# Performance work log

Hardware: AMD Instinct MI355X
Metric: run time of the kernel (lower is better)

Reference implementation:

```python
import jax, jax.numpy as jnp
import numpy as np

KR = 3  # kernel_range, SHIFT = 1


def _neighborhood(x):
    """x: [B,H,W,C] -> [B,H,W,9,C] stacking the 3x3 shifted views (zero pad),
    in the same (i,j) raster order as the original loop."""
    B, H, W, C = x.shape
    xp = jnp.pad(x, ((0, 0), (1, 1), (1, 1), (0, 0)))
    views = [xp[:, 1 + i:1 + i + H, 1 + j:1 + j + W, :]
             for i in (-1, 0, 1) for j in (-1, 0, 1)]
    return jnp.stack(views, axis=3)


def _conv(x, w, b):
    # tf.nn.conv2d NHWC, HWIO, SAME, stride 1
    return jax.lax.conv_general_dilated(
        x, w, window_strides=(1, 1), padding='SAME',
        dimension_numbers=('NHWC', 'HWIO', 'NHWC')) + b


def setup_inputs() -> dict:
    key = jax.random.key(0)
    ks = jax.random.split(key, 10)
    B, H, W, D = 8, 128, 128, 64
    g = lambda k, shape, fan: jax.random.normal(k, shape, jnp.float32) * np.float32(1.0 / np.sqrt(fan))
    return {
        'x': jax.random.normal(ks[0], (B, H, W, D), jnp.float32),
        'Q_P': g(ks[1], (D, D), D),
        'K_P': g(ks[2], (D, D), D),
        'V_P': g(ks[3], (D, D), D),
        'ff1_kernel': g(ks[4], (3, 3, D, D), 9 * D),
        'ff1_bias': jax.random.normal(ks[5], (D,), jnp.float32) * 0.01,
        'ff2_kernel': g(ks[6], (3, 3, D, 2 * D), 9 * D),
        'ff2_bias': jax.random.normal(ks[7], (2 * D,), jnp.float32) * 0.01,
        'ff3_kernel': g(ks[8], (3, 3, 2 * D, D), 9 * 2 * D),
        'ff3_bias': jax.random.normal(ks[9], (D,), jnp.float32) * 0.01,
    }


def reference(x, Q_P, K_P, V_P, ff1_kernel, ff1_bias, ff2_kernel, ff2_bias,
              ff3_kernel, ff3_bias):
    B, H, W, D = x.shape
    # 3x3 neighborhood gather (zero padded) and validity mask
    stk = _neighborhood(x)                                   # [B,H,W,9,D]
    mask = _neighborhood(jnp.ones((B, H, W, 1), x.dtype))    # [B,H,W,9,1]
    mask = mask[..., 0]                                      # [B,H,W,9]

    q = jnp.einsum('bhwd,de->bhwe', x, Q_P)                  # [B,H,W,D]
    k = jnp.einsum('bhwkd,de->bhwke', stk, K_P)              # [B,H,W,9,D]
    v = jnp.einsum('bhwkd,de->bhwke', stk, V_P)              # [B,H,W,9,D]

    # NOTE: faithful to original -- scores are MULTIPLIED by the mask
    # (masked entries become 0, not -inf) before softmax over the 9 neighbors.
    scores = jnp.einsum('bhwke,bhwe->bhwk', k, q) * mask     # [B,H,W,9]
    alpha = jax.nn.softmax(scores, axis=-1)
    attn = jnp.einsum('bhwk,bhwke->bhwe', alpha, v)          # [B,H,W,D]

    t = x + attn
    t_in = t
    t = jax.nn.relu(_conv(t, ff1_kernel, ff1_bias))
    t = jax.nn.relu(_conv(t, ff2_kernel, ff2_bias))
    t = jax.nn.relu(_conv(t, ff3_kernel, ff3_bias))
    return t_in + t
```

## Files before the change

### kernel.cpp

```cpp
#include <hip/hip_runtime.h>

typedef unsigned int uint32;
typedef unsigned short u16;
typedef short s16x8 __attribute__((ext_vector_type(8)));
typedef short s16x4 __attribute__((ext_vector_type(4)));
typedef float f32x4 __attribute__((ext_vector_type(4)));

#define DEVINL static __device__ __forceinline__
#define MFMA16(a, b, c) __builtin_amdgcn_mfma_f32_16x16x32_bf16(a, b, c, 0, 0, 0)

DEVINL float bf2f(u16 u){ return __uint_as_float(((uint32)u) << 16); }
DEVINL u16 f2bf(float f){
  uint32 u = __float_as_uint(f);
  u += 0x7fffu + ((u >> 16) & 1u);
  return (u16)(u >> 16);
}
DEVINL uint32 pack2(float a, float b){
  return (uint32)f2bf(a) | (((uint32)f2bf(b)) << 16);
}

__global__ void detect_k(const uint32* __restrict__ x, uint32* __restrict__ flag){
  const int lane = threadIdx.x;
  int sane = 0;
  for (int i = 0; i < 32; ++i){
    uint32 u = x[i * 64 + lane];
    uint32 e = (u >> 7) & 0xffu;
    sane += (e >= 100u && e <= 150u) ? 1 : 0;
  }
  for (int off = 32; off >= 1; off >>= 1) sane += __shfl_xor(sane, off);
  if (lane == 0) *flag = (sane > 1024) ? 1u : 0u;
}

template<int M>
__global__ void cvtall_k(const void* s0, const void* s1, const void* s2,
                         const void* s3, const void* s4, const void* s5,
                         const void* s6, const void* s7, const void* s8,
                         float* __restrict__ wb, const uint32* __restrict__ flag)
{
  if (*flag != (uint32)M) return;
  const int i = blockIdx.x * 256 + threadIdx.x;
  if (i >= 196864) return;
  const void* s; int j;
  if      (i < 4096)   { s = s0; j = i; }
  else if (i < 8192)   { s = s1; j = i - 4096; }
  else if (i < 12288)  { s = s2; j = i - 8192; }
  else if (i < 49152)  { s = s3; j = i - 12288; }
  else if (i < 49216)  { s = s4; j = i - 49152; }
  else if (i < 122944) { s = s5; j = i - 49216; }
  else if (i < 123072) { s = s6; j = i - 122944; }
  else if (i < 196800) { s = s7; j = i - 123072; }
  else                 { s = s8; j = i - 196800; }
  wb[i] = M ? bf2f(((const u16*)s)[j]) : ((const float*)s)[j];
}

__global__ __launch_bounds__(256)
void xcvt_k(const void* __restrict__ x, u16* __restrict__ xb,
            const uint32* __restrict__ flag)
{
  if (*flag != 0u) return;
  const size_t i0 = ((size_t)blockIdx.x * 256 + threadIdx.x) * 8;
  const float4 f0 = ((const float4*)x)[i0 / 4];
  const float4 f1 = ((const float4*)x)[i0 / 4 + 1];
  uint4 o;
  o.x = pack2(f0.x, f0.y); o.y = pack2(f0.z, f0.w);
  o.z = pack2(f1.x, f1.y); o.w = pack2(f1.z, f1.w);
  *(uint4*)(xb + i0) = o;
}

__global__ void gcomp_k(const float* __restrict__ wb, u16* __restrict__ gt){
  const int t = blockIdx.x * 256 + threadIdx.x;
  const int d = t >> 6, c = t & 63;
  const float* __restrict__ K = wb + 4096;
  const float* __restrict__ Q = wb;
  float s = 0.f;
#pragma unroll
  for (int e = 0; e < 64; ++e) s = fmaf(K[d * 64 + e], Q[c * 64 + e], s);
  const u16 hi = f2bf(s);
  gt[t] = hi;
  gt[4096 + t] = f2bf(s - bf2f(hi));
}

__global__ void pack_k(const float* __restrict__ wb, u16* __restrict__ bb){
  int i = blockIdx.x * 256 + threadIdx.x;
  if (i < 4096){
    const int o = i >> 6, c = i & 63;
    bb[8192 + i] = f2bf(wb[8192 + c * 64 + o]);
    return;
  }
  i -= 4096;
  if (i < 4096){
    const int o = i >> 6, c = i & 63;
    const float v = wb[8192 + c * 64 + o];
    bb[12288 + i] = f2bf(v - bf2f(f2bf(v)));
    return;
  }
  i -= 4096;
  if (i < 36864){
    const int chunk = i >> 11, rr = i & 2047, co = rr >> 5, kkp = rr & 31;
    const int slot = (kkp >> 3) ^ ((co >> 1) & 3), kk = slot * 8 + (kkp & 7);
    const int tap = chunk >> 1, ci = (chunk & 1) * 32 + kk;
    bb[16384 + i] = f2bf(wb[12288 + (tap * 64 + ci) * 64 + co]);
    return;
  }
  i -= 36864;
  if (i < 73728){
    const int half = i / 36864, i2 = i - half * 36864;
    const int chunk = i2 >> 11, rr = i2 & 2047, co = rr >> 5, kkp = rr & 31;
    const int slot = (kkp >> 3) ^ ((co >> 1) & 3), kk = slot * 8 + (kkp & 7);
    const int tap = chunk >> 1, ci = (chunk & 1) * 32 + kk;
    bb[53248 + i] = f2bf(wb[49216 + (tap * 64 + ci) * 128 + half * 64 + co]);
    return;
  }
  i -= 73728;
  {
    const int chunk = i >> 11, rr = i & 2047, co = rr >> 5, kkp = rr & 31;
    const int slot = (kkp >> 3) ^ ((co >> 1) & 3), kk = slot * 8 + (kkp & 7);
    const int tap = chunk >> 2, ci = (chunk & 3) * 32 + kk;
    bb[126976 + i] = f2bf(wb[123072 + (tap * 128 + ci) * 64 + co]);
  }
}

template<int ROWS, int CIN, int STRIDE>
DEVINL void stage_tile(const u16* __restrict__ img_base, int h0, int w0, u16* lds){
  constexpr int CH8 = CIN / 8;
  constexpr int NCH = ROWS * 66 * CH8;
  for (int idx = threadIdx.x; idx < NCH; idx += 256){
    const int row  = idx / (66 * CH8);
    const int rem  = idx - row * 66 * CH8;
    const int col  = rem / CH8;
    const int slot = rem - col * CH8;
    const int hi = h0 + row - 1, wi = w0 + col - 1;
    uint4 v = make_uint4(0u, 0u, 0u, 0u);
    if (hi >= 0 && hi < 128 && wi >= 0 && wi < 128)
      v = *(const uint4*)(img_base + (size_t)(hi * 128 + wi) * STRIDE + slot * 8);
    const int dst = (row * 66 + col) * CIN + ((slot ^ (col & 7)) << 3);
    *(uint4*)(lds + dst) = v;
  }
}

template<int COUT_FULL, bool RES, int MOUT>
DEVINL void conv_epilogue(f32x4 acc[4][4], u16* xh, const u16* __restrict__ res,
                          void* __restrict__ out, int img, int h0, int w0, int co0,
                          int wv, int l15, int lk)
{
  float* tl = (float*)xh;
  const int lane = threadIdx.x & 63;
#pragma unroll
  for (int pass = 0; pass < 2; ++pass){
    __syncthreads();
#pragma unroll
    for (int at2 = 0; at2 < 2; ++at2){
      const int at = pass * 2 + at2;
      const int pp = wv * 32 + at2 * 16 + lk * 4;
#pragma unroll
      for (int nt = 0; nt < 4; ++nt)
#pragma unroll
        for (int reg = 0; reg < 4; ++reg)
          tl[(pp + reg) * 72 + nt * 16 + l15] = fmaxf(acc[at][nt][reg], 0.f);
    }
    __syncthreads();
    const size_t rowpx = (size_t)img * 16384 + (size_t)(h0 + wv) * 128 + w0 + pass * 32;
    if (MOUT == 0){
#pragma unroll
      for (int k = 0; k < 8; ++k){
        const int px = k * 4 + (lane >> 4);
        const int c4 = (lane & 15) * 4;
        float4 v = *(const float4*)(tl + (wv * 32 + px) * 72 + c4);
        if (RES){
          const uint2 r = *(const uint2*)(res + (rowpx + px) * 64 + c4);
          v.x += bf2f((u16)(r.x & 0xffff)); v.y += bf2f((u16)(r.x >> 16));
          v.z += bf2f((u16)(r.y & 0xffff)); v.w += bf2f((u16)(r.y >> 16));
        }
        *(float4*)((float*)out + (rowpx + px) * 64 + c4) = v;
      }
    } else {
#pragma unroll
      for (int k = 0; k < 4; ++k){
        const int px = k * 8 + (lane >> 3);
        const int c8 = (lane & 7) * 8;
        const float* tp = tl + (wv * 32 + px) * 72 + c8;
        const float4 a = *(const float4*)tp;
        const float4 b = *(const float4*)(tp + 4);
        float v0=a.x, v1=a.y, v2=a.z, v3=a.w, v4=b.x, v5=b.y, v6=b.z, v7=b.w;
        if (RES){
          const uint4 r = *(const uint4*)(res + (rowpx + px) * 64 + c8);
          v0 += bf2f((u16)(r.x & 0xffff)); v1 += bf2f((u16)(r.x >> 16));
          v2 += bf2f((u16)(r.y & 0xffff)); v3 += bf2f((u16)(r.y >> 16));
          v4 += bf2f((u16)(r.z & 0xffff)); v5 += bf2f((u16)(r.z >> 16));
          v6 += bf2f((u16)(r.w & 0xffff)); v7 += bf2f((u16)(r.w >> 16));
        }
        uint4 o;
        o.x = pack2(v0, v1); o.y = pack2(v2, v3);
        o.z = pack2(v4, v5); o.w = pack2(v6, v7);
        *(uint4*)((u16*)out + (rowpx + px) * COUT_FULL + co0 + c8) = o;
      }
    }
  }
}

__global__ __launch_bounds__(256, 4)
void attn_mfma(const u16* __restrict__ xraw, const u16* __restrict__ xcv,
               const u16* __restrict__ gt, const u16* __restrict__ vt,
               u16* __restrict__ tb, const uint32* __restrict__ flag)
{
  __shared__ __align__(16) u16 xh[3 * 66 * 64];
  u16* yl  = xh;
  u16* yl2 = xh + 2 * 66 * 64;
  const int bx0 = blockIdx.x;
  const int bx = (bx0 & 7) * 256 + (bx0 >> 3);
  const int img = bx >> 8, h = (bx >> 1) & 127, w0 = (bx & 1) * 64;
  const int p0 = img * 16384 + h * 128 + w0;
  const u16* __restrict__ xsrc = (*flag != 0u) ? xraw : xcv;
  stage_tile<3, 64, 64>(xsrc + (size_t)img * 16384 * 64, h, w0, xh);
  __syncthreads();

  const int lane = threadIdx.x & 63, wv = threadIdx.x >> 6;
  const int l15 = lane & 15, lk = lane >> 4;
  const int pxm = wv * 16 + l15;

  f32x4 racc[4];
#pragma unroll
  for (int nt = 0; nt < 4; ++nt) racc[nt] = (f32x4){0.f, 0.f, 0.f, 0.f};
#pragma unroll
  for (int half = 0; half < 2; ++half){
#pragma unroll
    for (int ks = 0; ks < 2; ++ks){
      const int colq = pxm + 1;
      const int slot = ks * 4 + lk;
      const s16x8 bx_ = *(const s16x8*)&xh[(66 + colq) * 64 + ((slot ^ (colq & 7)) << 3)];
#pragma unroll
      for (int nt = 0; nt < 4; ++nt){
        const s16x8 ag = *(const s16x8*)(gt + half * 4096 +
                          (size_t)(nt * 16 + l15) * 64 + ks * 32 + lk * 8);
        racc[nt] = MFMA16(ag, bx_, racc[nt]);
      }
    }
  }

  float sc[9];
#pragma unroll
  for (int n = 0; n < 9; ++n){
    const int tr = n / 3, tc = n % 3;
    const int col = pxm + tc;
    const u16* xr = &xh[(tr * 66 + col) * 64];
    float s = 0.f;
#pragma unroll
    for (int nt = 0; nt < 4; ++nt){
      const int slot = nt * 2 + (lk >> 1);
      const s16x4 v = *(const s16x4*)&xr[((slot ^ (col & 7)) << 3) + (lk & 1) * 4];
#pragma unroll
      for (int j = 0; j < 4; ++j)
        s = fmaf(bf2f((u16)v[j]), racc[nt][j], s);
    }
    sc[n] = s;
  }
#pragma unroll
  for (int n = 0; n < 9; ++n){
    sc[n] += __shfl_xor(sc[n], 16);
    sc[n] += __shfl_xor(sc[n], 32);
  }

  float mx = sc[0];
#pragma unroll
  for (int n = 1; n < 9; ++n) mx = fmaxf(mx, sc[n]);
  float sum = 0.f;
#pragma unroll
  for (int n = 0; n < 9; ++n){
    const float e = __expf(sc[n] - mx);
    sc[n] = e; sum += e;
  }
  const float inv = 1.f / sum;
#pragma unroll
  for (int n = 0; n < 9; ++n) sc[n] *= inv;

  float y[16];
#pragma unroll
  for (int j = 0; j < 16; ++j) y[j] = 0.f;
#pragma unroll
  for (int n = 0; n < 9; ++n){
    const int tr = n / 3, tc = n % 3;
    const int col = pxm + tc;
    const u16* xr = &xh[(tr * 66 + col) * 64];
    const float a = sc[n];
#pragma unroll
    for (int sl = 0; sl < 2; ++sl){
      const int slot = lk * 2 + sl;
      const s16x8 v = *(const s16x8*)&xr[(slot ^ (col & 7)) << 3];
#pragma unroll
      for (int j = 0; j < 8; ++j)
        y[sl * 8 + j] = fmaf(a, bf2f((u16)v[j]), y[sl * 8 + j]);
    }
  }

  __syncthreads();

#pragma unroll
  for (int sl = 0; sl < 2; ++sl){
    uint32 hwd[4], lwd[4];
#pragma unroll
    for (int j = 0; j < 4; ++j){
      const float a = y[sl * 8 + 2 * j], b = y[sl * 8 + 2 * j + 1];
      const u16 ha = f2bf(a), hb = f2bf(b);
      hwd[j] = (uint32)ha | ((uint32)hb << 16);
      lwd[j] = (uint32)f2bf(a - bf2f(ha)) | ((uint32)f2bf(b - bf2f(hb)) << 16);
    }
    const int slot = lk * 2 + sl;
    const int off = pxm * 64 + ((slot ^ (pxm & 7)) << 3);
    *(uint4*)&yl [off] = make_uint4(hwd[0], hwd[1], hwd[2], hwd[3]);
    *(uint4*)&yl2[off] = make_uint4(lwd[0], lwd[1], lwd[2], lwd[3]);
  }

  __syncthreads();

  f32x4 tacc[4];
#pragma unroll
  for (int nt = 0; nt < 4; ++nt) tacc[nt] = (f32x4){0.f, 0.f, 0.f, 0.f};
#pragma unroll
  for (int half = 0; half < 2; ++half){
    const u16* yb = half ? yl2 : yl;
#pragma unroll
    for (int ks = 0; ks < 2; ++ks){
      const int px = wv * 16 + l15;
      const int slot = ks * 4 + lk;
      const s16x8 af = *(const s16x8*)&yb[px * 64 + ((slot ^ (px & 7)) << 3)];
#pragma unroll
      for (int nt = 0; nt < 4; ++nt){
        const s16x8 bf = *(const s16x8*)(vt + (size_t)(nt * 16 + l15) * 64 + ks * 32 + lk * 8);
        tacc[nt] = MFMA16(af, bf, tacc[nt]);
      }
    }
  }
#pragma unroll
  for (int nt = 0; nt < 4; ++nt){
#pragma unroll
    for (int reg = 0; reg < 4; ++reg){
      const int pxo = wv * 16 + lk * 4 + reg;
      const int co = nt * 16 + l15;
      const int col = pxo + 1;
      const int elem = (66 + col) * 64 + (((co >> 3) ^ (col & 7)) << 3) + (co & 7);
      tb[(size_t)(p0 + pxo) * 64 + co] = f2bf(bf2f(xh[elem]) + tacc[nt][reg]);
    }
  }
}

template<int COUT_FULL, bool RES, int MOUT>
__global__ __launch_bounds__(256)
void conv_mfma(const u16* __restrict__ in, const u16* __restrict__ wpk,
               const float* __restrict__ bias, const u16* __restrict__ res,
               void* __restrict__ out, const uint32* __restrict__ flag)
{
  if (MOUT >= 0){ if (*flag != (uint32)MOUT) return; }
  constexpr int TOT = 18;
  __shared__ __align__(16) u16 xh[6 * 66 * 64];
  __shared__ __align__(16) u16 Bb[3][2048];

  const int bx0 = blockIdx.x;
  const int bx  = (bx0 & 7) * 64 + (bx0 >> 3);
  const int img = bx >> 6;
  const int rem = bx & 63;
  const int h0  = (rem >> 1) * 4;
  const int w0  = (rem & 1) * 64;
  const int co0 = blockIdx.y * 64;
  const u16* __restrict__ wp = wpk + (size_t)blockIdx.y * TOT * 2048;

  auto stageB = [&](int it, int buf){
    const char* g = (const char*)(wp + (size_t)it * 2048) + threadIdx.x * 16;
    char* l = (char*)&Bb[buf][0] + threadIdx.x * 16;
    __builtin_amdgcn_global_load_lds((const __attribute__((address_space(1))) void*)g,
                                     (__attribute__((address_space(3))) void*)l, 16, 0, 0);
  };

  stage_tile<6, 64, 64>(in + (size_t)img * 16384 * 64, h0, w0, xh);
  stageB(0, 0);
  stageB(1, 1);
  __syncthreads();

  const int lane = threadIdx.x & 63, wv = threadIdx.x >> 6;
  const int l15 = lane & 15, lk = lane >> 4;

  f32x4 acc[4][4];
#pragma unroll
  for (int nt = 0; nt < 4; ++nt){
    const float b = bias[co0 + nt * 16 + l15];
#pragma unroll
    for (int at = 0; at < 4; ++at) acc[at][nt] = (f32x4){b, b, b, b};
  }

#pragma unroll 1
  for (int it = 0; it < TOT; ++it){
    if (it + 2 < TOT) stageB(it + 2, (it + 2) % 3);
    const int b = it % 3;
    const int tap = it >> 1, ks = it & 1;
    const int tr = tap / 3, tc = tap - tr * 3;
    const int slot = ks * 4 + lk;
    s16x8 av[4], bv[4];
#pragma unroll
    for (int at = 0; at < 4; ++at){
      const int col = at * 16 + l15 + tc;
      av[at] = *(const s16x8*)&xh[((wv + tr) * 66 + col) * 64 + ((slot ^ (col & 7)) << 3)];
    }
#pragma unroll
    for (int nt = 0; nt < 4; ++nt){
      const int co = nt * 16 + l15;
      bv[nt] = *(const s16x8*)&Bb[b][co * 32 + ((lk ^ ((co >> 1) & 3)) << 3)];
    }
#pragma unroll
    for (int at = 0; at < 4; ++at)
#pragma unroll
      for (int nt = 0; nt < 4; ++nt)
        acc[at][nt] = MFMA16(av[at], bv[nt], acc[at][nt]);

    if (it + 1 < TOT){
      if (it + 2 < TOT) asm volatile("s_waitcnt vmcnt(1)" ::: "memory");
      else              asm volatile("s_waitcnt vmcnt(0)" ::: "memory");
      __builtin_amdgcn_s_barrier();
      __builtin_amdgcn_sched_barrier(0);
    }
  }

  conv_epilogue<COUT_FULL, RES, MOUT>(acc, xh, res, out, img, h0, w0, co0, wv, l15, lk);
}

template<int MOUT>
__global__ __launch_bounds__(256)
void conv3_mfma(const u16* __restrict__ in, const u16* __restrict__ wpk,
                const float* __restrict__ bias, const u16* __restrict__ res,
                void* __restrict__ out, const uint32* __restrict__ flag)
{
  if (*flag != (uint32)MOUT) return;
  __shared__ __align__(16) u16 xh[6 * 66 * 64];
  __shared__ __align__(16) u16 Bb[3][2048];

  const int bx0 = blockIdx.x;
  const int bx  = (bx0 & 7) * 64 + (bx0 >> 3);
  const int img = bx >> 6;
  const int rem = bx & 63;
  const int h0  = (rem >> 1) * 4;
  const int w0  = (rem & 1) * 64;

  auto stageB = [&](int chunk, int buf){
    const char* g = (const char*)(wpk + (size_t)chunk * 2048) + threadIdx.x * 16;
    char* l = (char*)&Bb[buf][0] + threadIdx.x * 16;
    __builtin_amdgcn_global_load_lds((const __attribute__((address_space(1))) void*)g,
                                     (__attribute__((address_space(3))) void*)l, 16, 0, 0);
  };

  const int lane = threadIdx.x & 63, wv = threadIdx.x >> 6;
  const int l15 = lane & 15, lk = lane >> 4;

  auto chunkOf = [&](int it, int half){
    return ((it >> 1) << 2) + half * 2 + (it & 1);
  };

  f32x4 acc[4][4];
#pragma unroll
  for (int nt = 0; nt < 4; ++nt){
    const float b = bias[nt * 16 + l15];
#pragma unroll
    for (int at = 0; at < 4; ++at) acc[at][nt] = (f32x4){b, b, b, b};
  }

#pragma unroll 1
  for (int half = 0; half < 2; ++half){
    if (half) __syncthreads();
    stage_tile<6, 64, 128>(in + (size_t)img * 16384 * 128 + half * 64, h0, w0, xh);
    stageB(chunkOf(0, half), 0);
    stageB(chunkOf(1, half), 1);
    __syncthreads();

#pragma unroll 1
    for (int it = 0; it < 18; ++it){
      if (it + 2 < 18) stageB(chunkOf(it + 2, half), (it + 2) % 3);
      const int b = it % 3;
      const int tap = it >> 1, ks2 = it & 1;
      const int tr = tap / 3, tc = tap - tr * 3;
      const int slot = ks2 * 4 + lk;
      s16x8 av[4], bv[4];
#pragma unroll
      for (int at = 0; at < 4; ++at){
        const int col = at * 16 + l15 + tc;
        av[at] = *(const s16x8*)&xh[((wv + tr) * 66 + col) * 64 + ((slot ^ (col & 7)) << 3)];
      }
#pragma unroll
      for (int nt = 0; nt < 4; ++nt){
        const int co = nt * 16 + l15;
        bv[nt] = *(const s16x8*)&Bb[b][co * 32 + ((lk ^ ((co >> 1) & 3)) << 3)];
      }
#pragma unroll
      for (int at = 0; at < 4; ++at)
#pragma unroll
        for (int nt = 0; nt < 4; ++nt)
          acc[at][nt] = MFMA16(av[at], bv[nt], acc[at][nt]);

      if (it + 1 < 18){
        if (it + 2 < 18) asm volatile("s_waitcnt vmcnt(1)" ::: "memory");
        else             asm volatile("s_waitcnt vmcnt(0)" ::: "memory");
        __builtin_amdgcn_s_barrier();
        __builtin_amdgcn_sched_barrier(0);
      }
    }
  }

  conv_epilogue<64, true, MOUT>(acc, xh, res, out, img, h0, w0, 0, wv, l15, lk);
}

extern "C" void kernel_launch(void* const* d_in, const int* in_sizes, int n_in,
                              void* d_out, int out_size, void* d_ws, size_t ws_size,
                              hipStream_t stream)
{
  (void)in_sizes; (void)n_in; (void)out_size; (void)ws_size;

  char* ws = (char*)d_ws;
  float*  wblob = (float*)ws;
  uint32* flag  = (uint32*)(ws + 983040);
  u16*    bb    = (u16*)(ws + (1u << 20));
  u16*    gt   = bb;
  u16*    vt   = bb + 8192;
  u16*    w1pk = bb + 16384;
  u16*    w2pk = bb + 53248;
  u16*    w3pk = bb + 126976;

  u16*   c2 = (u16*)(ws + (size_t)2097152);
  u16*   tb = (u16*)(ws + (size_t)35651584);
  u16*   xb = (u16*)(ws + (size_t)52428800);
  u16*   c1 = (u16*)(ws + (size_t)52428800);

  detect_k<<<1, 64, 0, stream>>>((const uint32*)d_in[0], flag);

  cvtall_k<0><<<769, 256, 0, stream>>>(d_in[1], d_in[2], d_in[3], d_in[4], d_in[5],
                                       d_in[6], d_in[7], d_in[8], d_in[9], wblob, flag);
  cvtall_k<1><<<769, 256, 0, stream>>>(d_in[1], d_in[2], d_in[3], d_in[4], d_in[5],
                                       d_in[6], d_in[7], d_in[8], d_in[9], wblob, flag);

  xcvt_k<<<4096, 256, 0, stream>>>(d_in[0], xb, flag);

  gcomp_k<<<16, 256, 0, stream>>>(wblob, gt);
  pack_k<<<752, 256, 0, stream>>>(wblob, bb);

  attn_mfma<<<2048, 256, 0, stream>>>((const u16*)d_in[0], xb, gt, vt, tb, flag);

  conv_mfma<64, false, -1><<<dim3(512, 1), 256, 0, stream>>>(
      tb, w1pk, wblob + 49152, nullptr, c1, flag);
  conv_mfma<128, false, -1><<<dim3(512, 2), 256, 0, stream>>>(
      c1, w2pk, wblob + 122944, nullptr, c2, flag);
  conv3_mfma<0><<<512, 256, 0, stream>>>(
      c2, w3pk, wblob + 196800, tb, d_out, flag);
  conv3_mfma<1><<<512, 256, 0, stream>>>(
      c2, w3pk, wblob + 196800, tb, d_out, flag);
}
```

Before: 151.9 us.

## Keep conv weights resident in LDS and read activations directly from global

The conv kernels stop staging the halo input tile in LDS. They instead preload all 18 weight chunks per channel phase into LDS and load the A operands straight from global memory, with clamped addresses and zero masking for padding. This removes the per-iteration barriers and the triple-buffered weight pipeline, and merges conv3 into one templated kernel. In exchange the A operands come as uncoalesced per-lane global/L2 reads repeated across the 9 taps, and the LDS footprint grows to 72KB, which may lower occupancy.

```diff
diff --git a/kernel.cpp b/kernel.cpp
--- a/kernel.cpp
+++ b/kernel.cpp
@@ -139,11 +139,11 @@
 }
 
 template<int COUT_FULL, bool RES, int MOUT>
-DEVINL void conv_epilogue(f32x4 acc[4][4], u16* xh, const u16* __restrict__ res,
+DEVINL void conv_epilogue(f32x4 acc[4][4], u16* scratch, const u16* __restrict__ res,
                           void* __restrict__ out, int img, int h0, int w0, int co0,
                           int wv, int l15, int lk)
 {
-  float* tl = (float*)xh;
+  float* tl = (float*)scratch;
   const int lane = threadIdx.x & 63;
 #pragma unroll
   for (int pass = 0; pass < 2; ++pass){
@@ -343,16 +343,15 @@
   }
 }
 
-template<int COUT_FULL, bool RES, int MOUT>
+template<int CIN, int COUT_FULL, bool RES, int MOUT>
 __global__ __launch_bounds__(256)
-void conv_mfma(const u16* __restrict__ in, const u16* __restrict__ wpk,
+void conv_bres(const u16* __restrict__ in, const u16* __restrict__ wpk,
                const float* __restrict__ bias, const u16* __restrict__ res,
                void* __restrict__ out, const uint32* __restrict__ flag)
 {
   if (MOUT >= 0){ if (*flag != (uint32)MOUT) return; }
-  constexpr int TOT = 18;
-  __shared__ __align__(16) u16 xh[6 * 66 * 64];
-  __shared__ __align__(16) u16 Bb[3][2048];
+  constexpr int PH = CIN / 64;
+  __shared__ __align__(16) u16 Bb[18 * 2048];
 
   const int bx0 = blockIdx.x;
   const int bx  = (bx0 & 7) * 64 + (bx0 >> 3);
@@ -361,19 +360,8 @@
   const int h0  = (rem >> 1) * 4;
   const int w0  = (rem & 1) * 64;
   const int co0 = blockIdx.y * 64;
-  const u16* __restrict__ wp = wpk + (size_t)blockIdx.y * TOT * 2048;
-
-  auto stageB = [&](int it, int buf){
-    const char* g = (const char*)(wp + (size_t)it * 2048) + threadIdx.x * 16;
-    char* l = (char*)&Bb[buf][0] + threadIdx.x * 16;
-    __builtin_amdgcn_global_load_lds((const __attribute__((address_space(1))) void*)g,
-                                     (__attribute__((address_space(3))) void*)l, 16, 0, 0);
-  };
-
-  stage_tile<6, 64, 64>(in + (size_t)img * 16384 * 64, h0, w0, xh);
-  stageB(0, 0);
-  stageB(1, 1);
-  __syncthreads();
+  const u16* __restrict__ wp = wpk + (size_t)blockIdx.y * (18 * PH) * 2048;
+  const u16* __restrict__ ib = in + (size_t)img * 16384 * CIN;
 
   const int lane = threadIdx.x & 63, wv = threadIdx.x >> 6;
   const int l15 = lane & 15, lk = lane >> 4;
@@ -386,122 +374,52 @@
     for (int at = 0; at < 4; ++at) acc[at][nt] = (f32x4){b, b, b, b};
   }
 
-#pragma unroll 1
-  for (int it = 0; it < TOT; ++it){
-    if (it + 2 < TOT) stageB(it + 2, (it + 2) % 3);
-    const int b = it % 3;
-    const int tap = it >> 1, ks = it & 1;
-    const int tr = tap / 3, tc = tap - tr * 3;
-    const int slot = ks * 4 + lk;
-    s16x8 av[4], bv[4];
-#pragma unroll
-    for (int at = 0; at < 4; ++at){
-      const int col = at * 16 + l15 + tc;
-      av[at] = *(const s16x8*)&xh[((wv + tr) * 66 + col) * 64 + ((slot ^ (col & 7)) << 3)];
-    }
-#pragma unroll
-    for (int nt = 0; nt < 4; ++nt){
-      const int co = nt * 16 + l15;
-      bv[nt] = *(const s16x8*)&Bb[b][co * 32 + ((lk ^ ((co >> 1) & 3)) << 3)];
-    }
-#pragma unroll
-    for (int at = 0; at < 4; ++at)
-#pragma unroll
-      for (int nt = 0; nt < 4; ++nt)
-        acc[at][nt] = MFMA16(av[at], bv[nt], acc[at][nt]);
-
-    if (it + 1 < TOT){
-      if (it + 2 < TOT) asm volatile("s_waitcnt vmcnt(1)" ::: "memory");
-      else              asm volatile("s_waitcnt vmcnt(0)" ::: "memory");
-      __builtin_amdgcn_s_barrier();
-      __builtin_amdgcn_sched_barrier(0);
-    }
-  }
-
-  conv_epilogue<COUT_FULL, RES, MOUT>(acc, xh, res, out, img, h0, w0, co0, wv, l15, lk);
-}
-
-template<int MOUT>
-__global__ __launch_bounds__(256)
-void conv3_mfma(const u16* __restrict__ in, const u16* __restrict__ wpk,
-                const float* __restrict__ bias, const u16* __restrict__ res,
-                void* __restrict__ out, const uint32* __restrict__ flag)
-{
-  if (*flag != (uint32)MOUT) return;
-  __shared__ __align__(16) u16 xh[6 * 66 * 64];
-  __shared__ __align__(16) u16 Bb[3][2048];
-
-  const int bx0 = blockIdx.x;
-  const int bx  = (bx0 & 7) * 64 + (bx0 >> 3);
-  const int img = bx >> 6;
-  const int rem = bx & 63;
-  const int h0  = (rem >> 1) * 4;
-  const int w0  = (rem & 1) * 64;
-
-  auto stageB = [&](int chunk, int buf){
-    const char* g = (const char*)(wpk + (size_t)chunk * 2048) + threadIdx.x * 16;
-    char* l = (char*)&Bb[buf][0] + threadIdx.x * 16;
-    __builtin_amdgcn_global_load_lds((const __attribute__((address_space(1))) void*)g,
-                                     (__attribute__((address_space(3))) void*)l, 16, 0, 0);
-  };
-
-  const int lane = threadIdx.x & 63, wv = threadIdx.x >> 6;
-  const int l15 = lane & 15, lk = lane >> 4;
-
-  auto chunkOf = [&](int it, int half){
-    return ((it >> 1) << 2) + half * 2 + (it & 1);
-  };
-
-  f32x4 acc[4][4];
-#pragma unroll
-  for (int nt = 0; nt < 4; ++nt){
-    const float b = bias[nt * 16 + l15];
-#pragma unroll
-    for (int at = 0; at < 4; ++at) acc[at][nt] = (f32x4){b, b, b, b};
-  }
-
-#pragma unroll 1
-  for (int half = 0; half < 2; ++half){
-    if (half) __syncthreads();
-    stage_tile<6, 64, 128>(in + (size_t)img * 16384 * 128 + half * 64, h0, w0, xh);
-    stageB(chunkOf(0, half), 0);
-    stageB(chunkOf(1, half), 1);
+#pragma unroll
+  for (int ph = 0; ph < PH; ++ph){
+    if (ph) __syncthreads();
+#pragma unroll
+    for (int c = 0; c < 18; ++c){
+      const int ck = ((c >> 1) * 2 * PH) + ph * 2 + (c & 1);
+      const char* g = (const char*)(wp + (size_t)ck * 2048) + threadIdx.x * 16;
+      char* l = (char*)Bb + c * 4096 + threadIdx.x * 16;
+      __builtin_amdgcn_global_load_lds((const __attribute__((address_space(1))) void*)g,
+                                       (__attribute__((address_space(3))) void*)l, 16, 0, 0);
+    }
     __syncthreads();
 
-#pragma unroll 1
+    const int koff = ph * 64 + lk * 8;
+#pragma unroll 2
     for (int it = 0; it < 18; ++it){
-      if (it + 2 < 18) stageB(chunkOf(it + 2, half), (it + 2) % 3);
-      const int b = it % 3;
-      const int tap = it >> 1, ks2 = it & 1;
+      const int tap = it >> 1, ks = it & 1;
       const int tr = tap / 3, tc = tap - tr * 3;
-      const int slot = ks2 * 4 + lk;
+      const int rowi = h0 + wv + tr - 1;
+      const int rowc = min(max(rowi, 0), 127);
+      const bool rok = (rowi == rowc);
       s16x8 av[4], bv[4];
 #pragma unroll
       for (int at = 0; at < 4; ++at){
-        const int col = at * 16 + l15 + tc;
-        av[at] = *(const s16x8*)&xh[((wv + tr) * 66 + col) * 64 + ((slot ^ (col & 7)) << 3)];
+        const int colg = w0 + at * 16 + l15 + tc - 1;
+        const int colc = min(max(colg, 0), 127);
+        const bool ok = rok & (colg == colc);
+        uint4 u = *(const uint4*)(ib + (size_t)(rowc * 128 + colc) * CIN + koff + ks * 32);
+        u.x = ok ? u.x : 0u; u.y = ok ? u.y : 0u;
+        u.z = ok ? u.z : 0u; u.w = ok ? u.w : 0u;
+        av[at] = *(const s16x8*)&u;
       }
 #pragma unroll
       for (int nt = 0; nt < 4; ++nt){
         const int co = nt * 16 + l15;
-        bv[nt] = *(const s16x8*)&Bb[b][co * 32 + ((lk ^ ((co >> 1) & 3)) << 3)];
+        bv[nt] = *(const s16x8*)&Bb[it * 2048 + co * 32 + ((lk ^ ((co >> 1) & 3)) << 3)];
       }
 #pragma unroll
       for (int at = 0; at < 4; ++at)
 #pragma unroll
         for (int nt = 0; nt < 4; ++nt)
           acc[at][nt] = MFMA16(av[at], bv[nt], acc[at][nt]);
-
-      if (it + 1 < 18){
-        if (it + 2 < 18) asm volatile("s_waitcnt vmcnt(1)" ::: "memory");
-        else             asm volatile("s_waitcnt vmcnt(0)" ::: "memory");
-        __builtin_amdgcn_s_barrier();
-        __builtin_amdgcn_sched_barrier(0);
-      }
-    }
-  }
-
-  conv_epilogue<64, true, MOUT>(acc, xh, res, out, img, h0, w0, 0, wv, l15, lk);
+    }
+  }
+
+  conv_epilogue<COUT_FULL, RES, MOUT>(acc, Bb, res, out, img, h0, w0, co0, wv, l15, lk);
 }
 
 extern "C" void kernel_launch(void* const* d_in, const int* in_sizes, int n_in,
@@ -539,12 +457,12 @@
 
   attn_mfma<<<2048, 256, 0, stream>>>((const u16*)d_in[0], xb, gt, vt, tb, flag);
 
-  conv_mfma<64, false, -1><<<dim3(512, 1), 256, 0, stream>>>(
+  conv_bres<64, 64, false, -1><<<dim3(512, 1), 256, 0, stream>>>(
       tb, w1pk, wblob + 49152, nullptr, c1, flag);
-  conv_mfma<128, false, -1><<<dim3(512, 2), 256, 0, stream>>>(
+  conv_bres<64, 128, false, -1><<<dim3(512, 2), 256, 0, stream>>>(
       c1, w2pk, wblob + 122944, nullptr, c2, flag);
-  conv3_mfma<0><<<512, 256, 0, stream>>>(
+  conv_bres<128, 64, true, 0><<<dim3(512, 1), 256, 0, stream>>>(
       c2, w3pk, wblob + 196800, tb, d_out, flag);
-  conv3_mfma<1><<<512, 256, 0, stream>>>(
+  conv_bres<128, 64, true, 1><<<dim3(512, 1), 256, 0, stream>>>(
       c2, w3pk, wblob + 196800, tb, d_out, flag);
 }
```

Measured after the change: 174.9 us. 15.2% more time.
